# Kernel optimization log

Hardware: AMD Instinct MI355X
Metric: run time of the kernel (lower is better)

The kernel has to match this reference:

```python
import jax, jax.numpy as jnp
import numpy as np

NHEAD = 8

def setup_inputs() -> dict:
    key = jax.random.key(0)
    ks = jax.random.split(key, 6)
    b, n, d = 4, 1024, 512
    emb = jax.random.normal(ks[0], (b, n, d), dtype=jnp.float32)
    dirs = jax.random.normal(ks[1], (b, n, n, 3), dtype=jnp.float32)
    d_mask = jax.random.normal(ks[2], (b * NHEAD, n, n), dtype=jnp.float32) * 0.1
    W_proj = jax.random.normal(ks[3], (d, 3 * d), dtype=jnp.float32) / np.sqrt(d)
    b_proj = jnp.zeros((3 * d,), dtype=jnp.float32)
    w_force = jax.random.normal(ks[4], (d,), dtype=jnp.float32) / np.sqrt(d)
    b_force = jnp.zeros((1,), dtype=jnp.float32)
    return {"emb": emb, "dirs": dirs, "d_mask": d_mask, "W_proj": W_proj,
            "b_proj": b_proj, "w_force": w_force, "b_force": b_force}

def reference(emb, dirs, d_mask, W_proj, b_proj, w_force, b_force):
    b, n, d = emb.shape
    h = NHEAD
    dh = d // h
    scale = jnp.asarray(np.sqrt(d), emb.dtype)
    qkv = emb @ W_proj + b_proj                      # (b,n,3d)
    q, k, v = jnp.split(qkv, 3, axis=-1)
    q = q.reshape(b, n, h, dh).transpose(0, 2, 1, 3) / scale   # (b,h,n,dh)
    k = k.reshape(b, n, h, dh).transpose(0, 2, 1, 3)           # (b,h,n,dh)
    v = v.reshape(b, n, h, dh).transpose(0, 2, 1, 3)           # (b,h,n,dh)
    scores = jnp.einsum('bhid,bhjd->bhij', q, k) + d_mask.reshape(b, h, n, n)
    attn = jax.nn.softmax(scores, axis=-1)                     # (b,h,n,n); dropout in eval mode = identity
    # torch: (attn[...,None] * dirs[:,None]) @ v  materializes (b,h,n,n,3);
    # fused einsum computes the same per-axis weighted sum without it.
    xyz = jnp.einsum('bhij,bija,bhjd->biahd', attn, dirs, v)   # (b,n,3,h,dh)
    xyz = xyz.reshape(b, n, 3, d)
    out = jnp.einsum('bnad,d->bna', xyz, w_force) + b_force[0]  # (b,n,3)
    return out
```

## Files before the change

kernel.cpp:

```cpp
#include <hip/hip_runtime.h>
#include <hip/hip_bf16.h>

#define NH 8
#define BB 4
#define NN 1024
#define DD 512
#define DH 64
#define SCS 1032

typedef __bf16 bf16x8 __attribute__((ext_vector_type(8)));
typedef float f32x4 __attribute__((ext_vector_type(4)));

__device__ __forceinline__ unsigned short f2bf(float f) {
    union { float f; unsigned u; } v; v.f = f;
    unsigned u = v.u;
    unsigned r = u + 0x7FFFu + ((u >> 16) & 1u);
    return (unsigned short)(r >> 16);
}
__device__ __forceinline__ float b2f(unsigned short u) {
    union { unsigned u; float f; } cv; cv.u = ((unsigned)u) << 16; return cv.f;
}

__global__ __launch_bounds__(256) void k_prep(const float* __restrict__ W,
                                              const float* __restrict__ b_proj,
                                              const float* __restrict__ w_force,
                                              unsigned short* __restrict__ Wt,
                                              float* __restrict__ bias_eff,
                                              float* __restrict__ wv_eff,
                                              float* __restrict__ s_bias) {
    __shared__ float tile[32][33];
    int bx = blockIdx.x;
    int t = threadIdx.x;
    const float rscale = 0.044194173824159216f;
    if (bx < 512) {
        int c0 = (bx & 15) * 32;
        int n0 = (bx >> 4) * 32;
        for (int i = 0; i < 4; ++i) {
            int idx = t + i * 256;
            int r = idx >> 5, cn = idx & 31;
            tile[r][cn] = W[(c0 + r) * (3 * DD) + n0 + cn];
        }
        __syncthreads();
        for (int i = 0; i < 4; ++i) {
            int idx = t + i * 256;
            int nn = idx >> 5, cc = idx & 31;
            float v = tile[cc][nn];
            int n = n0 + nn;
            if (n < DD) v *= rscale;
            Wt[n * DD + c0 + cc] = f2bf(v);
        }
        if ((bx & 15) == 0 && t < 32) {
            int n = n0 + t;
            bias_eff[n] = b_proj[n] * (n < DD ? rscale : 1.0f);
        }
        return;
    }
    int wave = t >> 6, lane = t & 63;
    if (bx == 640) {
        if (wave == 0) {
            for (int hh = 0; hh < NH; ++hh) {
                float p = b_proj[2 * DD + hh * DH + lane] * w_force[hh * DH + lane];
                for (int off = 32; off; off >>= 1) p += __shfl_xor(p, off);
                if (lane == 0) s_bias[hh] = p;
            }
        }
        return;
    }
    int c = (bx - 512) * 4 + wave;
    const float* wr = W + (size_t)c * (3 * DD) + 2 * DD;
    #pragma unroll
    for (int hh = 0; hh < NH; ++hh) {
        float p = wr[hh * DH + lane] * w_force[hh * DH + lane];
        for (int off = 32; off; off >>= 1) p += __shfl_xor(p, off);
        if (lane == 0) wv_eff[c * 8 + hh] = p;
    }
}

__global__ __launch_bounds__(128) void k_s(const float* __restrict__ emb,
                                           const float* __restrict__ wv_eff,
                                           const float* __restrict__ s_bias,
                                           float* __restrict__ s_ws) {
    int t = blockIdx.x * 128 + threadIdx.x;
    int row = t >> 3;
    int h = t & 7;
    const float* er = emb + (size_t)row * DD;
    const float* wp = wv_eff + h;
    float acc = 0.f;
    #pragma unroll 8
    for (int c4 = 0; c4 < DD / 4; ++c4) {
        float4 e = *(const float4*)(er + c4 * 4);
        acc += e.x * wp[(c4 * 4 + 0) * 8];
        acc += e.y * wp[(c4 * 4 + 1) * 8];
        acc += e.z * wp[(c4 * 4 + 2) * 8];
        acc += e.w * wp[(c4 * 4 + 3) * 8];
    }
    int b = row >> 10, j = row & 1023;
    s_ws[(b * 8 + h) * NN + j] = acc + s_bias[h];
}

__global__ __launch_bounds__(256) void k_gemm(const float* __restrict__ emb,
                                              const unsigned short* __restrict__ Wt,
                                              const float* __restrict__ bias_eff,
                                              unsigned short* __restrict__ qb,
                                              unsigned short* __restrict__ kb) {
    __shared__ __align__(16) unsigned short a_s[128 * 32];
    __shared__ __align__(16) unsigned short b_s[128 * 32];
    int m0 = blockIdx.x * 128, n0 = blockIdx.y * 128;
    int t = threadIdx.x;
    int wave = t >> 6, lane = t & 63;
    int wr = (wave >> 1) * 64, wc = (wave & 1) * 64;
    int qd = lane >> 4, c = lane & 15;
    int sr = t >> 2, sg = (t & 3) * 8;
    f32x4 acc[4][4] = {};
    for (int k0 = 0; k0 < DD; k0 += 32) {
        float4 x0 = *(const float4*)(emb + (size_t)(m0 + sr) * DD + k0 + sg);
        float4 x1 = *(const float4*)(emb + (size_t)(m0 + sr) * DD + k0 + sg + 4);
        float4 y0 = *(const float4*)(emb + (size_t)(m0 + 64 + sr) * DD + k0 + sg);
        float4 y1 = *(const float4*)(emb + (size_t)(m0 + 64 + sr) * DD + k0 + sg + 4);
        uint4 bv0 = *(const uint4*)(Wt + (size_t)(n0 + sr) * DD + k0 + sg);
        uint4 bv1 = *(const uint4*)(Wt + (size_t)(n0 + 64 + sr) * DD + k0 + sg);
        union { unsigned short u[8]; uint4 v; } px, py;
        px.u[0] = f2bf(x0.x); px.u[1] = f2bf(x0.y); px.u[2] = f2bf(x0.z); px.u[3] = f2bf(x0.w);
        px.u[4] = f2bf(x1.x); px.u[5] = f2bf(x1.y); px.u[6] = f2bf(x1.z); px.u[7] = f2bf(x1.w);
        py.u[0] = f2bf(y0.x); py.u[1] = f2bf(y0.y); py.u[2] = f2bf(y0.z); py.u[3] = f2bf(y0.w);
        py.u[4] = f2bf(y1.x); py.u[5] = f2bf(y1.y); py.u[6] = f2bf(y1.z); py.u[7] = f2bf(y1.w);
        __syncthreads();
        *(uint4*)(&a_s[sr * 32 + sg]) = px.v;
        *(uint4*)(&a_s[(64 + sr) * 32 + sg]) = py.v;
        *(uint4*)(&b_s[sr * 32 + sg]) = bv0;
        *(uint4*)(&b_s[(64 + sr) * 32 + sg]) = bv1;
        __syncthreads();
        bf16x8 af[4], bfr[4];
        #pragma unroll
        for (int mi = 0; mi < 4; ++mi)
            af[mi] = *(const bf16x8*)(&a_s[(wr + mi * 16 + c) * 32 + qd * 8]);
        #pragma unroll
        for (int ni = 0; ni < 4; ++ni)
            bfr[ni] = *(const bf16x8*)(&b_s[(wc + ni * 16 + c) * 32 + qd * 8]);
        #pragma unroll
        for (int mi = 0; mi < 4; ++mi)
            #pragma unroll
            for (int ni = 0; ni < 4; ++ni)
                acc[mi][ni] = __builtin_amdgcn_mfma_f32_16x16x32_bf16(af[mi], bfr[ni], acc[mi][ni], 0, 0, 0);
    }
    bool isQ = (n0 < DD);
    unsigned short* dst = isQ ? qb : kb;
    int nb = isQ ? n0 : n0 - DD;
    #pragma unroll
    for (int mi = 0; mi < 4; ++mi)
        #pragma unroll
        for (int ni = 0; ni < 4; ++ni) {
            int col = nb + wc + ni * 16 + c;
            float be = bias_eff[isQ ? col : col + DD];
            #pragma unroll
            for (int r = 0; r < 4; ++r) {
                int row = m0 + wr + mi * 16 + qd * 4 + r;
                dst[(size_t)row * DD + col] = f2bf(acc[mi][ni][r] + be);
            }
        }
}

__global__ __launch_bounds__(256) void k_attn(const unsigned short* __restrict__ qb,
                                              const unsigned short* __restrict__ kb,
                                              const float* __restrict__ s_ws,
                                              const float* __restrict__ d_mask,
                                              const float* __restrict__ dirs,
                                              float* __restrict__ part) {
    __shared__ unsigned short sc_s[8 * SCS];
    int blk = blockIdx.x;
    int itile = blk & 127;
    int bh = blk >> 7;
    int h = bh & 7;
    int b = bh >> 3;
    int i0 = itile * 8;
    int t = threadIdx.x;
    int w = t >> 6, lane = t & 63, qd = lane >> 4, c = lane & 15;

    const unsigned short* qbase =
        qb + ((size_t)(b * NN + i0 + (c & 7)) * DD + h * DH + qd * 8);
    bf16x8 aq0 = *(const bf16x8*)(qbase);
    bf16x8 aq1 = *(const bf16x8*)(qbase + 32);
    int j0w = w * 256;
    #pragma unroll
    for (int jt = 0; jt < 16; ++jt) {
        int j0 = j0w + jt * 16;
        const unsigned short* kba =
            kb + ((size_t)(b * NN + j0 + c) * DD + h * DH + qd * 8);
        bf16x8 kf0 = *(const bf16x8*)(kba);
        bf16x8 kf1 = *(const bf16x8*)(kba + 32);
        f32x4 sc = {0.f, 0.f, 0.f, 0.f};
        sc = __builtin_amdgcn_mfma_f32_16x16x32_bf16(kf0, aq0, sc, 0, 0, 0);
        sc = __builtin_amdgcn_mfma_f32_16x16x32_bf16(kf1, aq1, sc, 0, 0, 0);
        ushort4 pk;
        pk.x = f2bf(sc[0]); pk.y = f2bf(sc[1]); pk.z = f2bf(sc[2]); pk.w = f2bf(sc[3]);
        if (c < 8)
            *(ushort4*)(&sc_s[c * SCS + j0 + qd * 4]) = pk;
    }
    __syncthreads();

    const float* sm = s_ws + bh * NN;
    float4 sv[4];
    #pragma unroll
    for (int seg = 0; seg < 4; ++seg)
        sv[seg] = *(const float4*)(sm + seg * 256 + lane * 4);

    const float* mbase = d_mask + (size_t)bh * NN * NN;
    const float* dbase = dirs + (size_t)b * NN * NN * 3;

    #pragma unroll
    for (int r2 = 0; r2 < 2; ++r2) {
        int il = w * 2 + r2;
        int i = i0 + il;
        const float* mrow = mbase + (size_t)i * NN + lane * 4;
        const float* drow = dbase + ((size_t)i * NN + lane * 4) * 3;
        float l = 0.f, a0 = 0.f, a1 = 0.f, a2 = 0.f;
        #pragma unroll
        for (int seg = 0; seg < 4; ++seg) {
            float4 mk = *(const float4*)(mrow + seg * 256);
            float4 d0 = *(const float4*)(drow + seg * 768);
            float4 d1 = *(const float4*)(drow + seg * 768 + 4);
            float4 d2 = *(const float4*)(drow + seg * 768 + 8);
            ushort4 scv = *(const ushort4*)(&sc_s[il * SCS + seg * 256 + lane * 4]);
            float p0 = __expf(b2f(scv.x) + mk.x);
            float p1 = __expf(b2f(scv.y) + mk.y);
            float p2 = __expf(b2f(scv.z) + mk.z);
            float p3 = __expf(b2f(scv.w) + mk.w);
            l += p0 + p1 + p2 + p3;
            float t0 = p0 * sv[seg].x, t1 = p1 * sv[seg].y;
            float t2 = p2 * sv[seg].z, t3 = p3 * sv[seg].w;
            a0 += t0 * d0.x + t1 * d0.w + t2 * d1.z + t3 * d2.y;
            a1 += t0 * d0.y + t1 * d1.x + t2 * d1.w + t3 * d2.z;
            a2 += t0 * d0.z + t1 * d1.y + t2 * d2.x + t3 * d2.w;
        }
        #pragma unroll
        for (int off = 1; off < 64; off <<= 1) {
            l  += __shfl_xor(l, off);
            a0 += __shfl_xor(a0, off);
            a1 += __shfl_xor(a1, off);
            a2 += __shfl_xor(a2, off);
        }
        if (lane == 0) {
            f32x4 o; o[0] = l; o[1] = a0; o[2] = a1; o[3] = a2;
            *(f32x4*)(part + ((size_t)bh * NN + i) * 4) = o;
        }
    }
}

__global__ __launch_bounds__(256) void k_fin(const float4* __restrict__ part,
                                             const float* __restrict__ b_force,
                                             float* __restrict__ out) {
    int t = blockIdx.x * 256 + threadIdx.x;
    int b = t >> 10, i = t & 1023;
    float o0, o1, o2;
    o0 = o1 = o2 = b_force[0];
    #pragma unroll
    for (int h = 0; h < NH; ++h) {
        float4 p = part[(((size_t)(b * NH + h)) << 10) + i];
        float inv = 1.0f / p.x;
        o0 += p.y * inv; o1 += p.z * inv; o2 += p.w * inv;
    }
    out[t * 3 + 0] = o0;
    out[t * 3 + 1] = o1;
    out[t * 3 + 2] = o2;
}

extern "C" void kernel_launch(void* const* d_in, const int* in_sizes, int n_in,
                              void* d_out, int out_size, void* d_ws, size_t ws_size,
                              hipStream_t stream) {
    (void)in_sizes; (void)n_in; (void)out_size; (void)ws_size;
    const float* emb     = (const float*)d_in[0];
    const float* dirs    = (const float*)d_in[1];
    const float* d_mask  = (const float*)d_in[2];
    const float* W       = (const float*)d_in[3];
    const float* b_proj  = (const float*)d_in[4];
    const float* w_force = (const float*)d_in[5];
    const float* b_force = (const float*)d_in[6];
    float* out = (float*)d_out;

    char* ws = (char*)d_ws;
    float* wv_eff   = (float*)ws;
    float* s_bias   = wv_eff + 4096;
    float* bias_eff = s_bias + 8;
    float* s_ws     = bias_eff + 1024;
    unsigned short* Wt = (unsigned short*)(s_ws + 32768);
    unsigned short* qb = Wt + 1024 * 512;
    unsigned short* kb = qb + 4096 * 512;
    float* part = (float*)(kb + 4096 * 512);

    hipLaunchKernelGGL(k_prep, dim3(641),      dim3(256), 0, stream,
                       W, b_proj, w_force, Wt, bias_eff, wv_eff, s_bias);
    hipLaunchKernelGGL(k_s,    dim3(256),      dim3(128), 0, stream, emb, wv_eff, s_bias, s_ws);
    hipLaunchKernelGGL(k_gemm, dim3(32, 8),    dim3(256), 0, stream, emb, Wt, bias_eff, qb, kb);
    hipLaunchKernelGGL(k_attn, dim3(BB * NH * 128), dim3(256), 0, stream,
                       qb, kb, s_ws, d_mask, dirs, part);
    hipLaunchKernelGGL(k_fin,  dim3(16),       dim3(256), 0, stream, (const float4*)part, b_force, out);
}
```

Measured before the change: 344.3 us.

## Split attention into QK score kernel and per-row softmax kernel sharing dirs across heads

The fused attention kernel is split in two. A QK kernel writes bf16 scores for two batches at a time to a global scratch buffer. A softmax/direction kernel then has one block per query row with one wavefront per head, so all 8 heads read the same dirs row together and dirs traffic is shared instead of reread per head. The cost is writing and reading a 16 MB bf16 score buffer per batch pair, plus extra kernel launches and a larger workspace.

```diff
diff --git a/kernel.cpp b/kernel.cpp
--- a/kernel.cpp
+++ b/kernel.cpp
@@ -6,7 +6,6 @@
 #define NN 1024
 #define DD 512
 #define DH 64
-#define SCS 1032
 
 typedef __bf16 bf16x8 __attribute__((ext_vector_type(8)));
 typedef float f32x4 __attribute__((ext_vector_type(4)));
@@ -160,26 +159,28 @@
         }
 }
 
-__global__ __launch_bounds__(256) void k_attn(const unsigned short* __restrict__ qb,
-                                              const unsigned short* __restrict__ kb,
-                                              const float* __restrict__ s_ws,
-                                              const float* __restrict__ d_mask,
-                                              const float* __restrict__ dirs,
-                                              float* __restrict__ part) {
-    __shared__ unsigned short sc_s[8 * SCS];
-    int blk = blockIdx.x;
-    int itile = blk & 127;
-    int bh = blk >> 7;
-    int h = bh & 7;
-    int b = bh >> 3;
-    int i0 = itile * 8;
+__global__ __launch_bounds__(256) void k_qk(const unsigned short* __restrict__ qb,
+                                            const unsigned short* __restrict__ kb,
+                                            unsigned short* __restrict__ sc,
+                                            int b0) {
+    int bx = blockIdx.x;
+    int bp = bx >> 7;
+    int h = (bx >> 4) & 7;
+    int itile = bx & 15;
+    int i0 = itile * 64;
+    int b = b0 + bp;
     int t = threadIdx.x;
     int w = t >> 6, lane = t & 63, qd = lane >> 4, c = lane & 15;
 
-    const unsigned short* qbase =
-        qb + ((size_t)(b * NN + i0 + (c & 7)) * DD + h * DH + qd * 8);
-    bf16x8 aq0 = *(const bf16x8*)(qbase);
-    bf16x8 aq1 = *(const bf16x8*)(qbase + 32);
+    bf16x8 aq0[4], aq1[4];
+    #pragma unroll
+    for (int s = 0; s < 4; ++s) {
+        const unsigned short* qbase =
+            qb + ((size_t)(b * NN + i0 + s * 16 + c) * DD + h * DH + qd * 8);
+        aq0[s] = *(const bf16x8*)(qbase);
+        aq1[s] = *(const bf16x8*)(qbase + 32);
+    }
+    unsigned short* scb = sc + ((size_t)(bp * NH + h)) * NN * NN;
     int j0w = w * 256;
     #pragma unroll
     for (int jt = 0; jt < 16; ++jt) {
@@ -188,61 +189,72 @@
             kb + ((size_t)(b * NN + j0 + c) * DD + h * DH + qd * 8);
         bf16x8 kf0 = *(const bf16x8*)(kba);
         bf16x8 kf1 = *(const bf16x8*)(kba + 32);
-        f32x4 sc = {0.f, 0.f, 0.f, 0.f};
-        sc = __builtin_amdgcn_mfma_f32_16x16x32_bf16(kf0, aq0, sc, 0, 0, 0);
-        sc = __builtin_amdgcn_mfma_f32_16x16x32_bf16(kf1, aq1, sc, 0, 0, 0);
-        ushort4 pk;
-        pk.x = f2bf(sc[0]); pk.y = f2bf(sc[1]); pk.z = f2bf(sc[2]); pk.w = f2bf(sc[3]);
-        if (c < 8)
-            *(ushort4*)(&sc_s[c * SCS + j0 + qd * 4]) = pk;
-    }
-    __syncthreads();
-
-    const float* sm = s_ws + bh * NN;
+        #pragma unroll
+        for (int s = 0; s < 4; ++s) {
+            f32x4 a = {0.f, 0.f, 0.f, 0.f};
+            a = __builtin_amdgcn_mfma_f32_16x16x32_bf16(kf0, aq0[s], a, 0, 0, 0);
+            a = __builtin_amdgcn_mfma_f32_16x16x32_bf16(kf1, aq1[s], a, 0, 0, 0);
+            ushort4 pk;
+            pk.x = f2bf(a[0]); pk.y = f2bf(a[1]); pk.z = f2bf(a[2]); pk.w = f2bf(a[3]);
+            *(ushort4*)(scb + (size_t)(i0 + s * 16 + c) * NN + j0 + qd * 4) = pk;
+        }
+    }
+}
+
+__global__ __launch_bounds__(512, 4) void k_soft(const unsigned short* __restrict__ sc,
+                                                 const float* __restrict__ s_ws,
+                                                 const float* __restrict__ d_mask,
+                                                 const float* __restrict__ dirs,
+                                                 float* __restrict__ part,
+                                                 int b0) {
+    int bx = blockIdx.x;
+    int bp = bx >> 10;
+    int i = bx & 1023;
+    int b = b0 + bp;
+    int t = threadIdx.x;
+    int h = t >> 6, lane = t & 63;
+    int bh = b * NH + h;
+
+    const float* sm = s_ws + (size_t)bh * NN;
     float4 sv[4];
     #pragma unroll
     for (int seg = 0; seg < 4; ++seg)
         sv[seg] = *(const float4*)(sm + seg * 256 + lane * 4);
 
-    const float* mbase = d_mask + (size_t)bh * NN * NN;
-    const float* dbase = dirs + (size_t)b * NN * NN * 3;
-
-    #pragma unroll
-    for (int r2 = 0; r2 < 2; ++r2) {
-        int il = w * 2 + r2;
-        int i = i0 + il;
-        const float* mrow = mbase + (size_t)i * NN + lane * 4;
-        const float* drow = dbase + ((size_t)i * NN + lane * 4) * 3;
-        float l = 0.f, a0 = 0.f, a1 = 0.f, a2 = 0.f;
-        #pragma unroll
-        for (int seg = 0; seg < 4; ++seg) {
-            float4 mk = *(const float4*)(mrow + seg * 256);
-            float4 d0 = *(const float4*)(drow + seg * 768);
-            float4 d1 = *(const float4*)(drow + seg * 768 + 4);
-            float4 d2 = *(const float4*)(drow + seg * 768 + 8);
-            ushort4 scv = *(const ushort4*)(&sc_s[il * SCS + seg * 256 + lane * 4]);
-            float p0 = __expf(b2f(scv.x) + mk.x);
-            float p1 = __expf(b2f(scv.y) + mk.y);
-            float p2 = __expf(b2f(scv.z) + mk.z);
-            float p3 = __expf(b2f(scv.w) + mk.w);
-            l += p0 + p1 + p2 + p3;
-            float t0 = p0 * sv[seg].x, t1 = p1 * sv[seg].y;
-            float t2 = p2 * sv[seg].z, t3 = p3 * sv[seg].w;
-            a0 += t0 * d0.x + t1 * d0.w + t2 * d1.z + t3 * d2.y;
-            a1 += t0 * d0.y + t1 * d1.x + t2 * d1.w + t3 * d2.z;
-            a2 += t0 * d0.z + t1 * d1.y + t2 * d2.x + t3 * d2.w;
-        }
-        #pragma unroll
-        for (int off = 1; off < 64; off <<= 1) {
-            l  += __shfl_xor(l, off);
-            a0 += __shfl_xor(a0, off);
-            a1 += __shfl_xor(a1, off);
-            a2 += __shfl_xor(a2, off);
-        }
-        if (lane == 0) {
-            f32x4 o; o[0] = l; o[1] = a0; o[2] = a1; o[3] = a2;
-            *(f32x4*)(part + ((size_t)bh * NN + i) * 4) = o;
-        }
+    const float* mrow = d_mask + ((size_t)bh * NN + i) * NN + lane * 4;
+    const float* drow = dirs + ((size_t)(b * NN + i) * NN + (size_t)(lane * 4)) * 3;
+    const unsigned short* scrow = sc + ((size_t)(bp * NH + h) * NN + i) * NN + lane * 4;
+
+    float l = 0.f, a0 = 0.f, a1 = 0.f, a2 = 0.f;
+    #pragma unroll
+    for (int seg = 0; seg < 4; ++seg) {
+        float4 mk = *(const float4*)(mrow + seg * 256);
+        float4 d0 = *(const float4*)(drow + seg * 768);
+        float4 d1 = *(const float4*)(drow + seg * 768 + 4);
+        float4 d2 = *(const float4*)(drow + seg * 768 + 8);
+        ushort4 scv = *(const ushort4*)(scrow + seg * 256);
+        float p0 = __expf(b2f(scv.x) + mk.x);
+        float p1 = __expf(b2f(scv.y) + mk.y);
+        float p2 = __expf(b2f(scv.z) + mk.z);
+        float p3 = __expf(b2f(scv.w) + mk.w);
+        l += p0 + p1 + p2 + p3;
+        float t0 = p0 * sv[seg].x, t1 = p1 * sv[seg].y;
+        float t2 = p2 * sv[seg].z, t3 = p3 * sv[seg].w;
+        a0 += t0 * d0.x + t1 * d0.w + t2 * d1.z + t3 * d2.y;
+        a1 += t0 * d0.y + t1 * d1.x + t2 * d1.w + t3 * d2.z;
+        a2 += t0 * d0.z + t1 * d1.y + t2 * d2.x + t3 * d2.w;
+    }
+
+    #pragma unroll
+    for (int off = 1; off < 64; off <<= 1) {
+        l  += __shfl_xor(l, off);
+        a0 += __shfl_xor(a0, off);
+        a1 += __shfl_xor(a1, off);
+        a2 += __shfl_xor(a2, off);
+    }
+    if (lane == 0) {
+        f32x4 o; o[0] = l; o[1] = a0; o[2] = a1; o[3] = a2;
+        *(f32x4*)(part + ((size_t)bh * NN + i) * 4) = o;
     }
 }
 
@@ -286,12 +298,16 @@
     unsigned short* qb = Wt + 1024 * 512;
     unsigned short* kb = qb + 4096 * 512;
     float* part = (float*)(kb + 4096 * 512);
+    unsigned short* scg = (unsigned short*)(part + 32 * 1024 * 4);
 
     hipLaunchKernelGGL(k_prep, dim3(641),      dim3(256), 0, stream,
                        W, b_proj, w_force, Wt, bias_eff, wv_eff, s_bias);
     hipLaunchKernelGGL(k_s,    dim3(256),      dim3(128), 0, stream, emb, wv_eff, s_bias, s_ws);
     hipLaunchKernelGGL(k_gemm, dim3(32, 8),    dim3(256), 0, stream, emb, Wt, bias_eff, qb, kb);
-    hipLaunchKernelGGL(k_attn, dim3(BB * NH * 128), dim3(256), 0, stream,
-                       qb, kb, s_ws, d_mask, dirs, part);
+    for (int pair = 0; pair < 2; ++pair) {
+        hipLaunchKernelGGL(k_qk,   dim3(256),  dim3(256), 0, stream, qb, kb, scg, pair * 2);
+        hipLaunchKernelGGL(k_soft, dim3(2048), dim3(512), 0, stream,
+                           scg, s_ws, d_mask, dirs, part, pair * 2);
+    }
     hipLaunchKernelGGL(k_fin,  dim3(16),       dim3(256), 0, stream, (const float4*)part, b_force, out);
 }
```

New measurement: 324.8 us. 5.7% less time.
